# Optimization experiments

Measured on AMD Instinct MI355X. Metric: run time of the kernel, lower is better.

## Reference

```python
import jax, jax.numpy as jnp
import numpy as np

N = 100000      # nodes
E = 1600000     # edges
F_IN = 64       # num_node_features
R = 8           # num_relations
G = 256         # graphs in batch
H, C = 4, 32    # GAT heads, per-head channels
NEG_SLOPE_ATT = 0.2    # GATConv attention leaky relu
NEG_SLOPE = 0.01       # F.leaky_relu default


def setup_inputs() -> dict:
    key = jax.random.key(0)
    ks = jax.random.split(key, 12)
    init = lambda k, shape, fan: (jax.random.normal(k, shape, jnp.float32) / np.sqrt(fan).astype(np.float32))
    x = jax.random.normal(ks[0], (N, F_IN), jnp.float32)
    edge_index = jax.random.randint(ks[1], (2, E), 0, N)
    edge_type = jax.random.randint(ks[2], (E,), 0, R)
    batch = (jnp.arange(N) * G) // N  # sorted graph ids, every segment non-empty
    return dict(
        x=x, edge_index=edge_index, edge_type=edge_type, batch=batch,
        gat_w=init(ks[3], (F_IN, H * C), F_IN),
        gat_att_src=init(ks[4], (H, C), C),
        gat_att_dst=init(ks[5], (H, C), C),
        gat_bias=jnp.zeros((H * C,), jnp.float32),
        dense1_w=init(ks[6], (H * C, 16), H * C),
        dense1_b=jnp.zeros((16,), jnp.float32),
        rw1=init(ks[7], (R, F_IN, 32), F_IN),
        root1=init(ks[8], (F_IN, 32), F_IN),
        rb1=jnp.zeros((32,), jnp.float32),
        rw2=init(ks[9], (R, 32, 16), 32),
        root2=init(ks[10], (32, 16), 32),
        rb2=jnp.zeros((16,), jnp.float32),
        dense_w=init(ks[11], (32, 1), 32),
        dense_b=jnp.zeros((1,), jnp.float32),
    )


def _gat(x, src, dst, w, att_src, att_dst, bias):
    h = (x @ w).reshape(N, H, C)                       # [N,H,C]
    a_src = jnp.sum(h * att_src, axis=-1)              # [N,H]
    a_dst = jnp.sum(h * att_dst, axis=-1)              # [N,H]
    e = jax.nn.leaky_relu(a_src[src] + a_dst[dst], NEG_SLOPE_ATT)  # [E,H]
    # segment softmax over incoming edges of each dst node
    m = jax.ops.segment_max(e, dst, num_segments=N)    # [N,H]
    p = jnp.exp(e - m[dst])
    s = jax.ops.segment_sum(p, dst, num_segments=N)    # [N,H]
    alpha = p / s[dst]
    msg = h[src] * alpha[:, :, None]                   # [E,H,C]
    out = jax.ops.segment_sum(msg, dst, num_segments=N)
    return out.reshape(N, H * C) + bias


def _rgcn(x, src, dst, edge_type, w, root, bias):
    # per-relation transform of all nodes, then edge gather (PyG RGCNConv, aggr='mean')
    xw = jnp.einsum('ni,rio->rno', x, w)               # [R,N,out]
    msg = xw[edge_type, src]                           # [E,out]
    comb = dst * R + edge_type                         # mean is per (dst, relation)
    cnt = jax.ops.segment_sum(jnp.ones((E,), x.dtype), comb, num_segments=N * R)
    agg = jax.ops.segment_sum(msg / cnt[comb][:, None], dst, num_segments=N)
    return agg + x @ root + bias


def reference(x, edge_index, edge_type, batch, gat_w, gat_att_src, gat_att_dst,
              gat_bias, dense1_w, dense1_b, rw1, root1, rb1, rw2, root2, rb2,
              dense_w, dense_b):
    src, dst = edge_index[0], edge_index[1]
    # GAT branch (dropout treated as identity / eval mode)
    h = _gat(x, src, dst, gat_w, gat_att_src, gat_att_dst, gat_bias)
    h = jax.nn.leaky_relu(h, NEG_SLOPE)
    h = jax.nn.leaky_relu(h @ dense1_w + dense1_b, NEG_SLOPE)
    gmax = jax.ops.segment_max(h, batch, num_segments=G)          # [G,16]
    # RGCN branch
    z = jax.nn.relu(_rgcn(x, src, dst, edge_type, rw1, root1, rb1))
    z = jax.nn.relu(_rgcn(z, src, dst, edge_type, rw2, root2, rb2))
    nodes_per_graph = jax.ops.segment_sum(jnp.ones((N,), x.dtype), batch, num_segments=G)
    gmean = jax.ops.segment_sum(z, batch, num_segments=G) / nodes_per_graph[:, None]
    # fuse
    zc = jnp.concatenate([gmax, gmean], axis=1)                   # [G,32]
    return zc @ dense_w + dense_b                                  # [G,1]
```

## Files before the change

kernel.cpp:

```cpp
#include <hip/hip_runtime.h>
#include <hip/hip_bf16.h>

typedef __hip_bfloat16 bf16;
typedef unsigned short u16;

#define N_NODES 100000
#define N_EDGES 1600000
#define F_IN 64
#define N_REL 8
#define N_GRAPH 256
#define N_HEAD 4
#define HC 128
#define NBLK_SCAN 391

__device__ __forceinline__ float lrelu(float x, float s) { return x >= 0.f ? x : s * x; }
__device__ __forceinline__ unsigned fenc(float f) {
  unsigned b = __float_as_uint(f);
  return (b & 0x80000000u) ? ~b : (b | 0x80000000u);
}
__device__ __forceinline__ float fdec(unsigned u) {
  float v = __uint_as_float((u & 0x80000000u) ? (u & 0x7fffffffu) : ~u);
  return fmaxf(fminf(v, 3e38f), -3e38f);
}
__device__ __forceinline__ float bf2f(bf16 v) { return __bfloat162float(v); }
__device__ __forceinline__ bf16 f2bf(float v) { return __float2bfloat16(v); }
__device__ __forceinline__ float lo_bf(unsigned u) { return __uint_as_float(u << 16); }
__device__ __forceinline__ float hi_bf(unsigned u) { return __uint_as_float(u & 0xFFFF0000u); }

template<bool BF> __device__ __forceinline__ float ldf(const void* p, size_t i) {
  if (BF) { u16 v = ((const u16*)p)[i]; return __uint_as_float(((unsigned)v) << 16); }
  else    { return ((const float*)p)[i]; }
}

__global__ void k_probe(const u16* __restrict__ xr, int* __restrict__ flag) {
  int t = threadIdx.x;
  int c = 0;
  for (int i = t; i < 1024; i += 256) {
    unsigned e = (xr[i] >> 7) & 0xFFu;
    if (e >= 100u && e <= 140u) c++;
  }
  __shared__ int sc[256];
  sc[t] = c;
  __syncthreads();
  for (int s = 128; s; s >>= 1) { if (t < s) sc[t] += sc[t + s]; __syncthreads(); }
  if (t == 0) *flag = (sc[0] >= 800) ? 1 : 0;
}

template<bool BF>
__device__ __forceinline__ void gat_h_body(const void* x, const void* w, const void* att_s,
                                           const void* att_d, bf16* __restrict__ h,
                                           float* __restrict__ a_src, float* __restrict__ a_dst) {
  int n = blockIdx.x, j = threadIdx.x;
  __shared__ float xs[F_IN];
  if (j < F_IN) xs[j] = ldf<BF>(x, (size_t)n * F_IN + j);
  __syncthreads();
  float acc = 0.f;
#pragma unroll
  for (int k = 0; k < F_IN; ++k) acc += xs[k] * ldf<BF>(w, (size_t)k * HC + j);
  h[(size_t)n * HC + j] = f2bf(acc);
  float ps = acc * ldf<BF>(att_s, j);
  float pd = acc * ldf<BF>(att_d, j);
#pragma unroll
  for (int off = 16; off > 0; off >>= 1) {
    ps += __shfl_down(ps, off, 32);
    pd += __shfl_down(pd, off, 32);
  }
  if ((j & 31) == 0) {
    a_src[n * N_HEAD + (j >> 5)] = ps;
    a_dst[n * N_HEAD + (j >> 5)] = pd;
  }
}
__global__ void k_gat_h(const void* x, const void* w, const void* att_s, const void* att_d,
                        bf16* h, float* a_src, float* a_dst, const int* flag) {
  if (__builtin_amdgcn_readfirstlane(*flag)) gat_h_body<true>(x, w, att_s, att_d, h, a_src, a_dst);
  else gat_h_body<false>(x, w, att_s, att_d, h, a_src, a_dst);
}

__global__ void k_hist(const int* __restrict__ ei, const int* __restrict__ etype,
                       int* __restrict__ deg, int* __restrict__ cnt) {
  int e = blockIdx.x * 256 + threadIdx.x;
  if (e >= N_EDGES) return;
  int d = ei[N_EDGES + e], t = etype[e];
  atomicAdd(&deg[d], 1);
  atomicAdd(&cnt[d * N_REL + t], 1);
}

__global__ void k_scan_a(const int* __restrict__ deg, int* __restrict__ rowptr,
                         int* __restrict__ scanblk) {
  __shared__ int buf[256];
  int tid = threadIdx.x;
  int i = blockIdx.x * 256 + tid;
  int v = (i < N_NODES) ? deg[i] : 0;
  buf[tid] = v;
  __syncthreads();
  for (int st = 1; st < 256; st <<= 1) {
    int t = buf[tid];
    int a = (tid >= st) ? buf[tid - st] : 0;
    __syncthreads();
    buf[tid] = t + a;
    __syncthreads();
  }
  if (i < N_NODES) rowptr[i] = buf[tid] - v;
  if (tid == 255) scanblk[blockIdx.x] = buf[255];
}
__global__ void k_scan_b(int* __restrict__ scanblk) {
  __shared__ int buf[512];
  int tid = threadIdx.x;
  int v = (tid < NBLK_SCAN) ? scanblk[tid] : 0;
  buf[tid] = v;
  __syncthreads();
  for (int st = 1; st < 512; st <<= 1) {
    int t = buf[tid];
    int a = (tid >= st) ? buf[tid - st] : 0;
    __syncthreads();
    buf[tid] = t + a;
    __syncthreads();
  }
  if (tid < NBLK_SCAN) scanblk[tid] = buf[tid] - v;
}
__global__ void k_scan_c(int* __restrict__ rowptr, int* __restrict__ wp,
                         const int* __restrict__ scanblk) {
  int i = blockIdx.x * 256 + threadIdx.x;
  if (i < N_NODES) {
    int val = rowptr[i] + scanblk[blockIdx.x];
    rowptr[i] = val;
    wp[i] = val;
  } else if (i == N_NODES) {
    rowptr[N_NODES] = N_EDGES;
  }
}

__global__ void k_scatter(const int* __restrict__ ei, const int* __restrict__ etype,
                          const float* __restrict__ a_src, const float* __restrict__ a_dst,
                          int* __restrict__ wp, unsigned* __restrict__ csr,
                          float4* __restrict__ p_logit) {
  int e = blockIdx.x * 256 + threadIdx.x;
  if (e >= N_EDGES) return;
  int sn = ei[e], d = ei[N_EDGES + e], t = etype[e];
  int pos = atomicAdd(&wp[d], 1);
  csr[pos] = (unsigned)sn | ((unsigned)t << 20);
  const float4 as = *(const float4*)&a_src[sn * 4];
  const float4 ad = *(const float4*)&a_dst[d * 4];
  float4 lg;
  lg.x = lrelu(as.x + ad.x, 0.2f);
  lg.y = lrelu(as.y + ad.y, 0.2f);
  lg.z = lrelu(as.z + ad.z, 0.2f);
  lg.w = lrelu(as.w + ad.w, 0.2f);
  p_logit[pos] = lg;
}

template<bool BF>
__device__ __forceinline__ void gat_agg_body(const int* __restrict__ rowptr,
                                             const unsigned* __restrict__ csr,
                                             const float* __restrict__ p_logit,
                                             const unsigned* __restrict__ hu, const void* gbias,
                                             const void* d1w, const void* d1b,
                                             const int* __restrict__ batch,
                                             unsigned* __restrict__ gmax, int* __restrict__ npg) {
  int tid = threadIdx.x;
  int wave = tid >> 6, l = tid & 63;
  int d = blockIdx.x * 4 + wave;
  __shared__ float os[4][132];
  int base = rowptr[d];
  int deg = rowptr[d + 1] - base;
  int head = l >> 4, slot = l & 15;
  float m = -1e30f;
  for (int i = slot; i < deg; i += 16) m = fmaxf(m, p_logit[(size_t)(base + i) * 4 + head]);
#pragma unroll
  for (int st = 1; st < 16; st <<= 1) m = fmaxf(m, __shfl_xor(m, st, 64));
  float s = 0.f;
  for (int i = slot; i < deg; i += 16) s += __expf(p_logit[(size_t)(base + i) * 4 + head] - m);
#pragma unroll
  for (int st = 1; st < 16; st <<= 1) s += __shfl_xor(s, st, 64);
  float si = (deg > 0) ? 1.f / s : 0.f;
  float acc0 = 0.f, acc1 = 0.f;
  int i = 0;
  for (; i + 4 <= deg; i += 4) {
    unsigned sp0 = csr[base + i], sp1 = csr[base + i + 1];
    unsigned sp2 = csr[base + i + 2], sp3 = csr[base + i + 3];
    float e0 = __expf(p_logit[(size_t)(base + i) * 4 + head] - m);
    float e1 = __expf(p_logit[(size_t)(base + i + 1) * 4 + head] - m);
    float e2 = __expf(p_logit[(size_t)(base + i + 2) * 4 + head] - m);
    float e3 = __expf(p_logit[(size_t)(base + i + 3) * 4 + head] - m);
    unsigned h0 = hu[(size_t)(sp0 & 0xFFFFF) * 64 + l];
    unsigned h1 = hu[(size_t)(sp1 & 0xFFFFF) * 64 + l];
    unsigned h2 = hu[(size_t)(sp2 & 0xFFFFF) * 64 + l];
    unsigned h3 = hu[(size_t)(sp3 & 0xFFFFF) * 64 + l];
    acc0 += lo_bf(h0) * e0 + lo_bf(h1) * e1 + lo_bf(h2) * e2 + lo_bf(h3) * e3;
    acc1 += hi_bf(h0) * e0 + hi_bf(h1) * e1 + hi_bf(h2) * e2 + hi_bf(h3) * e3;
  }
  for (; i < deg; ++i) {
    unsigned sp = csr[base + i];
    float e0 = __expf(p_logit[(size_t)(base + i) * 4 + head] - m);
    unsigned h0 = hu[(size_t)(sp & 0xFFFFF) * 64 + l];
    acc0 += lo_bf(h0) * e0;
    acc1 += hi_bf(h0) * e0;
  }
  acc0 *= si; acc1 *= si;
  os[wave][2 * l]     = lrelu(acc0 + ldf<BF>(gbias, 2 * l), 0.01f);
  os[wave][2 * l + 1] = lrelu(acc1 + ldf<BF>(gbias, 2 * l + 1), 0.01f);
  __syncthreads();
  if (tid < 64) {
    int node = tid >> 4, out = tid & 15;
    float a2 = ldf<BF>(d1b, out);
#pragma unroll
    for (int k = 0; k < HC; ++k) a2 += os[node][k] * ldf<BF>(d1w, (size_t)k * 16 + out);
    a2 = lrelu(a2, 0.01f);
    atomicMax(&gmax[batch[blockIdx.x * 4 + node] * 16 + out], fenc(a2));
  }
  if (tid < 4) atomicAdd(&npg[batch[blockIdx.x * 4 + tid]], 1);
}
__global__ void k_gat_agg(const int* rowptr, const unsigned* csr, const float* p_logit,
                          const bf16* h, const void* gbias, const void* d1w, const void* d1b,
                          const int* batch, unsigned* gmax, int* npg, const int* flag) {
  if (__builtin_amdgcn_readfirstlane(*flag))
    gat_agg_body<true>(rowptr, csr, p_logit, (const unsigned*)h, gbias, d1w, d1b, batch, gmax, npg);
  else
    gat_agg_body<false>(rowptr, csr, p_logit, (const unsigned*)h, gbias, d1w, d1b, batch, gmax, npg);
}

template<bool BF>
__device__ __forceinline__ void xw1_body(const void* x, const void* rw1, bf16* __restrict__ xw1) {
  __shared__ float xs[8][F_IN];
  int tid = threadIdx.x;
  int n0 = blockIdx.x * 8;
  for (int i = tid; i < 8 * F_IN; i += 256) {
    int nn = n0 + (i >> 6);
    xs[i >> 6][i & 63] = (nn < N_NODES) ? ldf<BF>(x, (size_t)nn * F_IN + (i & 63)) : 0.f;
  }
  __syncthreads();
  int nl = tid >> 5, c = tid & 31;
  int n = n0 + nl, r = blockIdx.y;
  float acc = 0.f;
#pragma unroll
  for (int k = 0; k < F_IN; ++k) acc += xs[nl][k] * ldf<BF>(rw1, (size_t)(r * F_IN + k) * 32 + c);
  if (n < N_NODES) xw1[((size_t)r * N_NODES + n) * 32 + c] = f2bf(acc);
}
__global__ void k_xw1(const void* x, const void* rw1, bf16* xw1, const int* flag) {
  if (__builtin_amdgcn_readfirstlane(*flag)) xw1_body<true>(x, rw1, xw1);
  else xw1_body<false>(x, rw1, xw1);
}

template<bool BF>
__device__ __forceinline__ void ragg1_body(const int* __restrict__ rowptr,
                                           const unsigned* __restrict__ csr,
                                           const int* __restrict__ cnt,
                                           const u16* __restrict__ xw, const void* x,
                                           const void* root1, const void* rb1,
                                           float* __restrict__ z1) {
  __shared__ float xs[4][F_IN];
  __shared__ float cinv[4][N_REL];
  int tid = threadIdx.x;
  int n0 = blockIdx.x * 4;
  {
    int nn = n0 + (tid >> 6);
    xs[tid >> 6][tid & 63] = ldf<BF>(x, (size_t)nn * F_IN + (tid & 63));
  }
  if (tid < 32) {
    int cv = cnt[(n0 + (tid >> 3)) * N_REL + (tid & 7)];
    cinv[tid >> 3][tid & 7] = (cv > 0) ? 1.f / (float)cv : 0.f;
  }
  __syncthreads();
  int wave = tid >> 6, l = tid & 63;
  int half = l >> 5, c = l & 31;
  int n = n0 + wave;
  int base = rowptr[n], deg = rowptr[n + 1] - base;
  float acc = 0.f;
  int i = half;
  for (; i + 2 < deg; i += 4) {
    unsigned sp0 = csr[base + i], sp1 = csr[base + i + 2];
    int t0 = sp0 >> 20, t1 = sp1 >> 20;
    u16 v0 = xw[((size_t)t0 * N_NODES + (sp0 & 0xFFFFF)) * 32 + c];
    u16 v1 = xw[((size_t)t1 * N_NODES + (sp1 & 0xFFFFF)) * 32 + c];
    acc += __uint_as_float(((unsigned)v0) << 16) * cinv[wave][t0];
    acc += __uint_as_float(((unsigned)v1) << 16) * cinv[wave][t1];
  }
  if (i < deg) {
    unsigned sp = csr[base + i];
    int t = sp >> 20;
    u16 v = xw[((size_t)t * N_NODES + (sp & 0xFFFFF)) * 32 + c];
    acc += __uint_as_float(((unsigned)v) << 16) * cinv[wave][t];
  }
  float r = 0.f;
#pragma unroll
  for (int kk = 0; kk < 32; ++kk) {
    int k = half * 32 + kk;
    r += xs[wave][k] * ldf<BF>(root1, (size_t)k * 32 + c);
  }
  float tot = acc + r;
  tot += __shfl_xor(tot, 32, 64);
  if (half == 0) z1[(size_t)n * 32 + c] = fmaxf(tot + ldf<BF>(rb1, c), 0.f);
}
__global__ void k_ragg1(const int* rowptr, const unsigned* csr, const int* cnt,
                        const bf16* xw1, const void* x, const void* root1, const void* rb1,
                        float* z1, const int* flag) {
  if (__builtin_amdgcn_readfirstlane(*flag))
    ragg1_body<true>(rowptr, csr, cnt, (const u16*)xw1, x, root1, rb1, z1);
  else
    ragg1_body<false>(rowptr, csr, cnt, (const u16*)xw1, x, root1, rb1, z1);
}

template<bool BF>
__device__ __forceinline__ void zw2_body(const float* __restrict__ z1, const void* rw2,
                                         bf16* __restrict__ zw2) {
  __shared__ float zs[16][32];
  int tid = threadIdx.x;
  int n0 = blockIdx.x * 16;
  for (int i = tid; i < 16 * 32; i += 256) {
    int nn = n0 + (i >> 5);
    zs[i >> 5][i & 31] = (nn < N_NODES) ? z1[(size_t)nn * 32 + (i & 31)] : 0.f;
  }
  __syncthreads();
  int nl = tid >> 4, c = tid & 15;
  int n = n0 + nl, r = blockIdx.y;
  float acc = 0.f;
#pragma unroll
  for (int k = 0; k < 32; ++k) acc += zs[nl][k] * ldf<BF>(rw2, (size_t)(r * 32 + k) * 16 + c);
  if (n < N_NODES) zw2[((size_t)r * N_NODES + n) * 16 + c] = f2bf(acc);
}
__global__ void k_zw2(const float* z1, const void* rw2, bf16* zw2, const int* flag) {
  if (__builtin_amdgcn_readfirstlane(*flag)) zw2_body<true>(z1, rw2, zw2);
  else zw2_body<false>(z1, rw2, zw2);
}

template<bool BF>
__device__ __forceinline__ void ragg2_body(const int* __restrict__ rowptr,
                                           const unsigned* __restrict__ csr,
                                           const int* __restrict__ cnt,
                                           const u16* __restrict__ zw,
                                           const float* __restrict__ z1, const void* root2,
                                           const void* rb2, const int* __restrict__ batch,
                                           float* __restrict__ gsum) {
  __shared__ float zs[4][33];
  __shared__ float cinv[4][N_REL];
  int tid = threadIdx.x;
  int n0 = blockIdx.x * 4;
  if (tid < 128) {
    int nn = n0 + (tid >> 5);
    zs[tid >> 5][tid & 31] = z1[(size_t)nn * 32 + (tid & 31)];
  }
  if (tid < 32) {
    int cv = cnt[(n0 + (tid >> 3)) * N_REL + (tid & 7)];
    cinv[tid >> 3][tid & 7] = (cv > 0) ? 1.f / (float)cv : 0.f;
  }
  __syncthreads();
  int wave = tid >> 6, l = tid & 63;
  int q = l >> 4, c = l & 15;
  int n = n0 + wave;
  int base = rowptr[n], deg = rowptr[n + 1] - base;
  float acc = 0.f;
  int i = q;
  for (; i + 4 < deg; i += 8) {
    unsigned sp0 = csr[base + i], sp1 = csr[base + i + 4];
    int t0 = sp0 >> 20, t1 = sp1 >> 20;
    u16 v0 = zw[((size_t)t0 * N_NODES + (sp0 & 0xFFFFF)) * 16 + c];
    u16 v1 = zw[((size_t)t1 * N_NODES + (sp1 & 0xFFFFF)) * 16 + c];
    acc += __uint_as_float(((unsigned)v0) << 16) * cinv[wave][t0];
    acc += __uint_as_float(((unsigned)v1) << 16) * cinv[wave][t1];
  }
  if (i < deg) {
    unsigned sp = csr[base + i];
    int t = sp >> 20;
    u16 v = zw[((size_t)t * N_NODES + (sp & 0xFFFFF)) * 16 + c];
    acc += __uint_as_float(((unsigned)v) << 16) * cinv[wave][t];
  }
  float r = 0.f;
#pragma unroll
  for (int kk = 0; kk < 8; ++kk) {
    int k = q * 8 + kk;
    r += zs[wave][k] * ldf<BF>(root2, (size_t)k * 16 + c);
  }
  float tot = acc + r;
  tot += __shfl_xor(tot, 16, 64);
  tot += __shfl_xor(tot, 32, 64);
  if (q == 0) {
    float z2 = fmaxf(tot + ldf<BF>(rb2, c), 0.f);
    atomicAdd(&gsum[batch[n] * 16 + c], z2);
  }
}
__global__ void k_ragg2(const int* rowptr, const unsigned* csr, const int* cnt,
                        const bf16* zw2, const float* z1, const void* root2, const void* rb2,
                        const int* batch, float* gsum, const int* flag) {
  if (__builtin_amdgcn_readfirstlane(*flag))
    ragg2_body<true>(rowptr, csr, cnt, (const u16*)zw2, z1, root2, rb2, batch, gsum);
  else
    ragg2_body<false>(rowptr, csr, cnt, (const u16*)zw2, z1, root2, rb2, batch, gsum);
}

template<bool BF>
__device__ __forceinline__ void final_body(const unsigned* __restrict__ gmax,
                                           const float* __restrict__ gsum,
                                           const int* __restrict__ npg, const void* dw,
                                           const void* db, void* out) {
  int g = threadIdx.x;
  if (g >= N_GRAPH) return;
  float acc = ldf<BF>(db, 0);
  int np = npg[g]; if (np < 1) np = 1;
  float inv = 1.f / (float)np;
#pragma unroll
  for (int c = 0; c < 16; ++c) {
    acc += fdec(gmax[g * 16 + c]) * ldf<BF>(dw, c);
    acc += (gsum[g * 16 + c] * inv) * ldf<BF>(dw, 16 + c);
  }
  if (BF) ((bf16*)out)[g] = f2bf(acc);
  else ((float*)out)[g] = acc;
}
__global__ void k_final(const unsigned* gmax, const float* gsum, const int* npg,
                        const void* dw, const void* db, void* out, const int* flag) {
  if (__builtin_amdgcn_readfirstlane(*flag)) final_body<true>(gmax, gsum, npg, dw, db, out);
  else final_body<false>(gmax, gsum, npg, dw, db, out);
}

extern "C" void kernel_launch(void* const* d_in, const int* in_sizes, int n_in,
                              void* d_out, int out_size, void* d_ws, size_t ws_size,
                              hipStream_t stream) {
  const void* x        = d_in[0];
  const int*  ei       = (const int*)d_in[1];
  const int*  etype    = (const int*)d_in[2];
  const int*  batch    = (const int*)d_in[3];
  const void* gat_w    = d_in[4];
  const void* att_src  = d_in[5];
  const void* att_dst  = d_in[6];
  const void* gat_bias = d_in[7];
  const void* d1w      = d_in[8];
  const void* d1b      = d_in[9];
  const void* rw1      = d_in[10];
  const void* root1    = d_in[11];
  const void* rb1      = d_in[12];
  const void* rw2      = d_in[13];
  const void* root2    = d_in[14];
  const void* rb2      = d_in[15];
  const void* dw       = d_in[16];
  const void* db       = d_in[17];

  char* ws = (char*)d_ws;
  const size_t o_h     = 0;
  const size_t o_plog  = 25600000;
  const size_t o_xw1   = 0;
  const size_t o_zw2   = 0;
  const size_t o_asrc  = 51200000;
  const size_t o_adst  = 52800000;
  const size_t o_deg   = 54400000;
  const size_t o_rowp  = 54800000;
  const size_t o_wp    = 55200016;
  const size_t o_cnt   = 55600032;
  const size_t o_csr   = 58800032;
  const size_t o_z1    = 65200032;
  const size_t o_sblk  = 78000032;
  const size_t o_gmax  = 78001600;
  const size_t o_gsum  = 78017984;
  const size_t o_npg   = 78034368;
  const size_t o_flag  = 78035392;
  const size_t total   = 78035396;
  if (ws_size < total) return;

  bf16*     h      = (bf16*)(ws + o_h);
  float*    plog   = (float*)(ws + o_plog);
  bf16*     xw1    = (bf16*)(ws + o_xw1);
  bf16*     zw2    = (bf16*)(ws + o_zw2);
  float*    a_src  = (float*)(ws + o_asrc);
  float*    a_dst  = (float*)(ws + o_adst);
  int*      deg    = (int*)(ws + o_deg);
  int*      rowptr = (int*)(ws + o_rowp);
  int*      wp     = (int*)(ws + o_wp);
  int*      cnt    = (int*)(ws + o_cnt);
  unsigned* csr    = (unsigned*)(ws + o_csr);
  float*    z1     = (float*)(ws + o_z1);
  int*      sblk   = (int*)(ws + o_sblk);
  unsigned* gmax   = (unsigned*)(ws + o_gmax);
  float*    gsum   = (float*)(ws + o_gsum);
  int*      npg    = (int*)(ws + o_npg);
  int*      flag   = (int*)(ws + o_flag);

  k_probe<<<1, 256, 0, stream>>>((const u16*)x, flag);

  hipMemsetAsync(ws + o_deg, 0, o_csr - o_deg, stream);
  hipMemsetAsync(ws + o_gmax, 0, 33792, stream);

  k_gat_h<<<N_NODES, 128, 0, stream>>>(x, gat_w, att_src, att_dst, h, a_src, a_dst, flag);

  k_hist<<<(N_EDGES + 255) / 256, 256, 0, stream>>>(ei, etype, deg, cnt);
  k_scan_a<<<NBLK_SCAN, 256, 0, stream>>>(deg, rowptr, sblk);
  k_scan_b<<<1, 512, 0, stream>>>(sblk);
  k_scan_c<<<NBLK_SCAN, 256, 0, stream>>>(rowptr, wp, sblk);
  k_scatter<<<(N_EDGES + 255) / 256, 256, 0, stream>>>(ei, etype, a_src, a_dst, wp, csr,
                                                       (float4*)plog);

  k_gat_agg<<<N_NODES / 4, 256, 0, stream>>>(rowptr, csr, plog, h, gat_bias, d1w, d1b, batch,
                                             gmax, npg, flag);

  k_xw1<<<dim3((N_NODES + 7) / 8, N_REL), 256, 0, stream>>>(x, rw1, xw1, flag);
  k_ragg1<<<N_NODES / 4, 256, 0, stream>>>(rowptr, csr, cnt, xw1, x, root1, rb1, z1, flag);

  k_zw2<<<dim3((N_NODES + 15) / 16, N_REL), 256, 0, stream>>>(z1, rw2, zw2, flag);
  k_ragg2<<<N_NODES / 4, 256, 0, stream>>>(rowptr, csr, cnt, zw2, z1, root2, rb2,
                                           batch, gsum, flag);

  k_final<<<1, 256, 0, stream>>>(gmax, gsum, npg, dw, db, d_out, flag);
}
```

Baseline: 1.315 ms.

## Precompute GAT softmax alphas in separate kernels and batch node GEMM per block

The per-destination segment softmax moves out of the GAT aggregation kernel into two new kernels. k_msum computes the per-node max and inverse sum, reusing the a_src/a_dst buffers. k_alpha then writes normalized alphas in place of the logits, using a new per-edge destination array filled by the scatter kernel. The aggregation loop drops its two logit passes and the exp work, and unrolls to 8 edges for more memory-level parallelism. Separately, k_gat_h now handles 8 nodes per block with the weight matrix cached in LDS as packed bf16. This trades two extra launches and extra edge-array traffic for a lighter gather loop, and slightly changes the rounding of h.

```diff
diff --git a/kernel.cpp b/kernel.cpp
--- a/kernel.cpp
+++ b/kernel.cpp
@@ -26,6 +26,10 @@
 __device__ __forceinline__ bf16 f2bf(float v) { return __float2bfloat16(v); }
 __device__ __forceinline__ float lo_bf(unsigned u) { return __uint_as_float(u << 16); }
 __device__ __forceinline__ float hi_bf(unsigned u) { return __uint_as_float(u & 0xFFFF0000u); }
+__device__ __forceinline__ unsigned f2bfu(float v) {
+  unsigned u = __float_as_uint(v);
+  return (u + 0x7FFFu + ((u >> 16) & 1u)) >> 16;
+}
 
 template<bool BF> __device__ __forceinline__ float ldf(const void* p, size_t i) {
   if (BF) { u16 v = ((const u16*)p)[i]; return __uint_as_float(((unsigned)v) << 16); }
@@ -48,30 +52,52 @@
 
 template<bool BF>
 __device__ __forceinline__ void gat_h_body(const void* x, const void* w, const void* att_s,
-                                           const void* att_d, bf16* __restrict__ h,
+                                           const void* att_d, u16* __restrict__ h,
                                            float* __restrict__ a_src, float* __restrict__ a_dst) {
-  int n = blockIdx.x, j = threadIdx.x;
-  __shared__ float xs[F_IN];
-  if (j < F_IN) xs[j] = ldf<BF>(x, (size_t)n * F_IN + j);
-  __syncthreads();
-  float acc = 0.f;
-#pragma unroll
-  for (int k = 0; k < F_IN; ++k) acc += xs[k] * ldf<BF>(w, (size_t)k * HC + j);
-  h[(size_t)n * HC + j] = f2bf(acc);
-  float ps = acc * ldf<BF>(att_s, j);
-  float pd = acc * ldf<BF>(att_d, j);
-#pragma unroll
-  for (int off = 16; off > 0; off >>= 1) {
-    ps += __shfl_down(ps, off, 32);
-    pd += __shfl_down(pd, off, 32);
-  }
-  if ((j & 31) == 0) {
-    a_src[n * N_HEAD + (j >> 5)] = ps;
-    a_dst[n * N_HEAD + (j >> 5)] = pd;
+  __shared__ unsigned wp[64 * 64];
+  __shared__ float xs[8][F_IN];
+  int tid = threadIdx.x;
+  int n0 = blockIdx.x * 8;
+  for (int i = tid; i < 4096; i += 256) {
+    if (BF) wp[i] = ((const unsigned*)w)[i];
+    else {
+      float a = ((const float*)w)[2 * i], b = ((const float*)w)[2 * i + 1];
+      wp[i] = (f2bfu(b) << 16) | f2bfu(a);
+    }
+  }
+  for (int i = tid; i < 8 * F_IN; i += 256)
+    xs[i >> 6][i & 63] = ldf<BF>(x, (size_t)(n0 + (i >> 6)) * F_IN + (i & 63));
+  __syncthreads();
+  int j = tid & 127, sub = tid >> 7;
+  float acc[4] = {0.f, 0.f, 0.f, 0.f};
+#pragma unroll
+  for (int k = 0; k < F_IN; ++k) {
+    unsigned wv = wp[k * 64 + (j >> 1)];
+    float wf = (j & 1) ? hi_bf(wv) : lo_bf(wv);
+#pragma unroll
+    for (int q = 0; q < 4; ++q) acc[q] += xs[sub * 4 + q][k] * wf;
+  }
+  float asj = ldf<BF>(att_s, j), adj = ldf<BF>(att_d, j);
+  int lane = tid & 63;
+#pragma unroll
+  for (int q = 0; q < 4; ++q) {
+    int nd = sub * 4 + q;
+    h[(size_t)(n0 + nd) * HC + j] = (u16)f2bfu(acc[q]);
+    float ps = acc[q] * asj, pd = acc[q] * adj;
+#pragma unroll
+    for (int off = 16; off > 0; off >>= 1) {
+      ps += __shfl_down(ps, off, 32);
+      pd += __shfl_down(pd, off, 32);
+    }
+    if ((lane & 31) == 0) {
+      int head = j >> 5;
+      a_src[(n0 + nd) * N_HEAD + head] = ps;
+      a_dst[(n0 + nd) * N_HEAD + head] = pd;
+    }
   }
 }
 __global__ void k_gat_h(const void* x, const void* w, const void* att_s, const void* att_d,
-                        bf16* h, float* a_src, float* a_dst, const int* flag) {
+                        u16* h, float* a_src, float* a_dst, const int* flag) {
   if (__builtin_amdgcn_readfirstlane(*flag)) gat_h_body<true>(x, w, att_s, att_d, h, a_src, a_dst);
   else gat_h_body<false>(x, w, att_s, att_d, h, a_src, a_dst);
 }
@@ -133,12 +159,13 @@
 __global__ void k_scatter(const int* __restrict__ ei, const int* __restrict__ etype,
                           const float* __restrict__ a_src, const float* __restrict__ a_dst,
                           int* __restrict__ wp, unsigned* __restrict__ csr,
-                          float4* __restrict__ p_logit) {
+                          float4* __restrict__ p_logit, int* __restrict__ dstarr) {
   int e = blockIdx.x * 256 + threadIdx.x;
   if (e >= N_EDGES) return;
   int sn = ei[e], d = ei[N_EDGES + e], t = etype[e];
   int pos = atomicAdd(&wp[d], 1);
   csr[pos] = (unsigned)sn | ((unsigned)t << 20);
+  dstarr[pos] = d;
   const float4 as = *(const float4*)&a_src[sn * 4];
   const float4 ad = *(const float4*)&a_dst[d * 4];
   float4 lg;
@@ -149,10 +176,46 @@
   p_logit[pos] = lg;
 }
 
+__global__ void k_msum(const int* __restrict__ rowptr, const float* __restrict__ p_logit,
+                       float* __restrict__ m_arr, float* __restrict__ si_arr) {
+  int tid = threadIdx.x;
+  int n = blockIdx.x * 16 + (tid >> 4);
+  int l16 = tid & 15, head = l16 & 3, slot = l16 >> 2;
+  int base = rowptr[n], deg = rowptr[n + 1] - base;
+  float m = -1e30f;
+  for (int i = slot; i < deg; i += 4) m = fmaxf(m, p_logit[(size_t)(base + i) * 4 + head]);
+  m = fmaxf(m, __shfl_xor(m, 4, 64));
+  m = fmaxf(m, __shfl_xor(m, 8, 64));
+  float s = 0.f;
+  for (int i = slot; i < deg; i += 4) s += __expf(p_logit[(size_t)(base + i) * 4 + head] - m);
+  s += __shfl_xor(s, 4, 64);
+  s += __shfl_xor(s, 8, 64);
+  if (slot == 0) {
+    m_arr[n * 4 + head] = m;
+    si_arr[n * 4 + head] = (deg > 0) ? 1.f / s : 0.f;
+  }
+}
+
+__global__ void k_alpha(const int* __restrict__ dstarr, const float* __restrict__ m_arr,
+                        const float* __restrict__ si_arr, float4* __restrict__ plog4) {
+  int p = blockIdx.x * 256 + threadIdx.x;
+  if (p >= N_EDGES) return;
+  int d = dstarr[p];
+  float4 lg = plog4[p];
+  const float4 m4 = *(const float4*)&m_arr[d * 4];
+  const float4 s4 = *(const float4*)&si_arr[d * 4];
+  float4 a;
+  a.x = __expf(lg.x - m4.x) * s4.x;
+  a.y = __expf(lg.y - m4.y) * s4.y;
+  a.z = __expf(lg.z - m4.z) * s4.z;
+  a.w = __expf(lg.w - m4.w) * s4.w;
+  plog4[p] = a;
+}
+
 template<bool BF>
 __device__ __forceinline__ void gat_agg_body(const int* __restrict__ rowptr,
                                              const unsigned* __restrict__ csr,
-                                             const float* __restrict__ p_logit,
+                                             const float* __restrict__ alpha,
                                              const unsigned* __restrict__ hu, const void* gbias,
                                              const void* d1w, const void* d1b,
                                              const int* __restrict__ batch,
@@ -163,40 +226,39 @@
   __shared__ float os[4][132];
   int base = rowptr[d];
   int deg = rowptr[d + 1] - base;
-  int head = l >> 4, slot = l & 15;
-  float m = -1e30f;
-  for (int i = slot; i < deg; i += 16) m = fmaxf(m, p_logit[(size_t)(base + i) * 4 + head]);
-#pragma unroll
-  for (int st = 1; st < 16; st <<= 1) m = fmaxf(m, __shfl_xor(m, st, 64));
-  float s = 0.f;
-  for (int i = slot; i < deg; i += 16) s += __expf(p_logit[(size_t)(base + i) * 4 + head] - m);
-#pragma unroll
-  for (int st = 1; st < 16; st <<= 1) s += __shfl_xor(s, st, 64);
-  float si = (deg > 0) ? 1.f / s : 0.f;
+  int head = l >> 4;
   float acc0 = 0.f, acc1 = 0.f;
   int i = 0;
-  for (; i + 4 <= deg; i += 4) {
+  for (; i + 8 <= deg; i += 8) {
+    unsigned sp[8]; float av[8]; unsigned hv[8];
+#pragma unroll
+    for (int k = 0; k < 8; ++k) sp[k] = csr[base + i + k];
+#pragma unroll
+    for (int k = 0; k < 8; ++k) av[k] = alpha[(size_t)(base + i + k) * 4 + head];
+#pragma unroll
+    for (int k = 0; k < 8; ++k) hv[k] = hu[(size_t)(sp[k] & 0xFFFFF) * 64 + l];
+#pragma unroll
+    for (int k = 0; k < 8; ++k) {
+      acc0 += lo_bf(hv[k]) * av[k];
+      acc1 += hi_bf(hv[k]) * av[k];
+    }
+  }
+  for (; i + 2 <= deg; i += 2) {
     unsigned sp0 = csr[base + i], sp1 = csr[base + i + 1];
-    unsigned sp2 = csr[base + i + 2], sp3 = csr[base + i + 3];
-    float e0 = __expf(p_logit[(size_t)(base + i) * 4 + head] - m);
-    float e1 = __expf(p_logit[(size_t)(base + i + 1) * 4 + head] - m);
-    float e2 = __expf(p_logit[(size_t)(base + i + 2) * 4 + head] - m);
-    float e3 = __expf(p_logit[(size_t)(base + i + 3) * 4 + head] - m);
+    float a0 = alpha[(size_t)(base + i) * 4 + head];
+    float a1 = alpha[(size_t)(base + i + 1) * 4 + head];
     unsigned h0 = hu[(size_t)(sp0 & 0xFFFFF) * 64 + l];
     unsigned h1 = hu[(size_t)(sp1 & 0xFFFFF) * 64 + l];
-    unsigned h2 = hu[(size_t)(sp2 & 0xFFFFF) * 64 + l];
-    unsigned h3 = hu[(size_t)(sp3 & 0xFFFFF) * 64 + l];
-    acc0 += lo_bf(h0) * e0 + lo_bf(h1) * e1 + lo_bf(h2) * e2 + lo_bf(h3) * e3;
-    acc1 += hi_bf(h0) * e0 + hi_bf(h1) * e1 + hi_bf(h2) * e2 + hi_bf(h3) * e3;
-  }
-  for (; i < deg; ++i) {
+    acc0 += lo_bf(h0) * a0 + lo_bf(h1) * a1;
+    acc1 += hi_bf(h0) * a0 + hi_bf(h1) * a1;
+  }
+  if (i < deg) {
     unsigned sp = csr[base + i];
-    float e0 = __expf(p_logit[(size_t)(base + i) * 4 + head] - m);
+    float a0 = alpha[(size_t)(base + i) * 4 + head];
     unsigned h0 = hu[(size_t)(sp & 0xFFFFF) * 64 + l];
-    acc0 += lo_bf(h0) * e0;
-    acc1 += hi_bf(h0) * e0;
-  }
-  acc0 *= si; acc1 *= si;
+    acc0 += lo_bf(h0) * a0;
+    acc1 += hi_bf(h0) * a0;
+  }
   os[wave][2 * l]     = lrelu(acc0 + ldf<BF>(gbias, 2 * l), 0.01f);
   os[wave][2 * l + 1] = lrelu(acc1 + ldf<BF>(gbias, 2 * l + 1), 0.01f);
   __syncthreads();
@@ -210,13 +272,13 @@
   }
   if (tid < 4) atomicAdd(&npg[batch[blockIdx.x * 4 + tid]], 1);
 }
-__global__ void k_gat_agg(const int* rowptr, const unsigned* csr, const float* p_logit,
-                          const bf16* h, const void* gbias, const void* d1w, const void* d1b,
+__global__ void k_gat_agg(const int* rowptr, const unsigned* csr, const float* alpha,
+                          const u16* h, const void* gbias, const void* d1w, const void* d1b,
                           const int* batch, unsigned* gmax, int* npg, const int* flag) {
   if (__builtin_amdgcn_readfirstlane(*flag))
-    gat_agg_body<true>(rowptr, csr, p_logit, (const unsigned*)h, gbias, d1w, d1b, batch, gmax, npg);
+    gat_agg_body<true>(rowptr, csr, alpha, (const unsigned*)h, gbias, d1w, d1b, batch, gmax, npg);
   else
-    gat_agg_body<false>(rowptr, csr, p_logit, (const unsigned*)h, gbias, d1w, d1b, batch, gmax, npg);
+    gat_agg_body<false>(rowptr, csr, alpha, (const unsigned*)h, gbias, d1w, d1b, batch, gmax, npg);
 }
 
 template<bool BF>
@@ -451,10 +513,11 @@
   const size_t o_gsum  = 78017984;
   const size_t o_npg   = 78034368;
   const size_t o_flag  = 78035392;
-  const size_t total   = 78035396;
+  const size_t o_dst   = 78035400;
+  const size_t total   = 84435400;
   if (ws_size < total) return;
 
-  bf16*     h      = (bf16*)(ws + o_h);
+  u16*      h      = (u16*)(ws + o_h);
   float*    plog   = (float*)(ws + o_plog);
   bf16*     xw1    = (bf16*)(ws + o_xw1);
   bf16*     zw2    = (bf16*)(ws + o_zw2);
@@ -471,20 +534,24 @@
   float*    gsum   = (float*)(ws + o_gsum);
   int*      npg    = (int*)(ws + o_npg);
   int*      flag   = (int*)(ws + o_flag);
+  int*      dstarr = (int*)(ws + o_dst);
 
   k_probe<<<1, 256, 0, stream>>>((const u16*)x, flag);
 
   hipMemsetAsync(ws + o_deg, 0, o_csr - o_deg, stream);
   hipMemsetAsync(ws + o_gmax, 0, 33792, stream);
 
-  k_gat_h<<<N_NODES, 128, 0, stream>>>(x, gat_w, att_src, att_dst, h, a_src, a_dst, flag);
+  k_gat_h<<<N_NODES / 8, 256, 0, stream>>>(x, gat_w, att_src, att_dst, h, a_src, a_dst, flag);
 
   k_hist<<<(N_EDGES + 255) / 256, 256, 0, stream>>>(ei, etype, deg, cnt);
   k_scan_a<<<NBLK_SCAN, 256, 0, stream>>>(deg, rowptr, sblk);
   k_scan_b<<<1, 512, 0, stream>>>(sblk);
   k_scan_c<<<NBLK_SCAN, 256, 0, stream>>>(rowptr, wp, sblk);
   k_scatter<<<(N_EDGES + 255) / 256, 256, 0, stream>>>(ei, etype, a_src, a_dst, wp, csr,
-                                                       (float4*)plog);
+                                                       (float4*)plog, dstarr);
+
+  k_msum<<<N_NODES / 16, 256, 0, stream>>>(rowptr, plog, a_src, a_dst);
+  k_alpha<<<(N_EDGES + 255) / 256, 256, 0, stream>>>(dstarr, a_src, a_dst, (float4*)plog);
 
   k_gat_agg<<<N_NODES / 4, 256, 0, stream>>>(rowptr, csr, plog, h, gat_bias, d1w, d1b, batch,
                                              gmax, npg, flag);
```

New measurement: 1.978 ms. +50.5%, slower.
